# Optimization experiments

Hardware: AMD Instinct MI355X
Metric: run time of the kernel (lower is better)

The kernel has to match this reference:

```python
import jax, jax.numpy as jnp
import numpy as np

B = 4           # batchsize == poolsize, pool = arange(B)
N_NODES = 32768
N_EDGES = 262144
CH_V = 16
CH_E = 16
HID = 64
CH_MSG = 2 * CH_V + CH_E  # 48


def setup_inputs() -> dict:
    key = jax.random.key(0)
    ks = jax.random.split(key, 8)
    node_vals = jax.random.normal(ks[0], (B, N_NODES, CH_V), jnp.float32) * 0.01
    edge_vals = jax.random.normal(ks[1], (B, N_EDGES, CH_E), jnp.float32) * 0.1
    conn_a = jax.random.randint(ks[2], (N_EDGES,), 0, N_NODES)
    conn_b = jax.random.randint(ks[3], (N_EDGES,), 0, N_NODES)
    w = lambda k, sh: jax.random.normal(k, sh, jnp.float32) * 0.1
    return {
        "node_vals": node_vals, "edge_vals": edge_vals,
        "conn_a": conn_a, "conn_b": conn_b,
        "Wm1": w(ks[4], (CH_MSG, HID)), "bm1": jnp.zeros((HID,), jnp.float32),
        "Wm2": w(ks[5], (HID, CH_MSG)), "bm2": jnp.zeros((CH_MSG,), jnp.float32),
        "Wu1": w(ks[6], (3 * CH_V, HID)), "bu1": jnp.zeros((HID,), jnp.float32),
        "Wu2": w(ks[7], (HID, CH_V)), "bu2": jnp.zeros((CH_V,), jnp.float32),
    }


def reference(node_vals, edge_vals, conn_a, conn_b,
              Wm1, bm1, Wm2, bm2, Wu1, bu1, Wu2, bu2):
    # NeuralGraph.timestep with node_dropout_p = edge_dropout_p = 0 (masks are identity),
    # use_update=True, average_messages=True, nodes=True, edges=True.
    h_a = node_vals[:, conn_a]                      # [B, E, CH_V] gather at source nodes
    h_b = node_vals[:, conn_b]                      # [B, E, CH_V] gather at target nodes
    h = jnp.concatenate([h_a, h_b, edge_vals], -1)  # [B, E, 48]
    # message MLP (Linear -> tanh -> Linear)
    m = jnp.tanh(h @ Wm1 + bm1) @ Wm2 + bm2         # [B, E, 48]
    m_a = m[..., :CH_V]
    m_b = m[..., CH_V:2 * CH_V]
    m_ab = m[..., 2 * CH_V:]
    # scatter-add aggregation per node (index_add_ along node dim)
    agg_a = jnp.zeros((B, N_NODES, CH_V), m.dtype).at[:, conn_a].add(m_a)
    agg_b = jnp.zeros((B, N_NODES, CH_V), m.dtype).at[:, conn_b].add(m_b)
    # count-based averaging (counts clamped to >= 1, matching the buffer fixup)
    ones = jnp.ones((N_EDGES,), m.dtype)
    cnt_a = jnp.maximum(jax.ops.segment_sum(ones, conn_a, num_segments=N_NODES), 1.0)
    cnt_b = jnp.maximum(jax.ops.segment_sum(ones, conn_b, num_segments=N_NODES), 1.0)
    agg_a = agg_a / cnt_a[None, :, None]
    agg_b = agg_b / cnt_b[None, :, None]
    # update MLP
    u_in = jnp.concatenate([agg_a, agg_b, node_vals], -1)   # [B, N, 48]
    updates = jnp.tanh(u_in @ Wu1 + bu1) @ Wu2 + bu2        # [B, N, CH_V]
    new_node_vals = node_vals + updates
    new_edge_vals = edge_vals + m_ab
    return new_node_vals, new_edge_vals
```

## Files before the change

kernel.cpp:

```cpp
#include <hip/hip_runtime.h>
#include <hip/hip_bf16.h>
#include <cstdint>
#include <cstddef>

#define B 4
#define NN 32768
#define NE 262144
#define CV 16
#define CE 16
#define HID 64
#define CM 48

using frag  = __attribute__((ext_vector_type(8))) short;
using f32x4 = __attribute__((ext_vector_type(4))) float;

__device__ __forceinline__ float fast_tanh(float x) {
    float e = __expf(2.0f * x);
    return 1.0f - 2.0f / (e + 1.0f);
}

__device__ __forceinline__ unsigned short f2bf(float x) {
    union { float f; unsigned u; } v; v.f = x;
    unsigned r = (v.u + 0x7FFFu + ((v.u >> 16) & 1u)) >> 16;
    return (unsigned short)r;
}

__device__ __forceinline__ float bf2f(unsigned short x) {
    union { unsigned u; float f; } v; v.u = ((unsigned)x) << 16;
    return v.f;
}

__device__ __forceinline__ unsigned pk2bf(float lo, float hi) {
    union { __hip_bfloat162 h; unsigned u; } v;
    v.h = __float22bfloat162_rn(make_float2(lo, hi));
    return v.u;
}

__device__ __forceinline__ unsigned swo(int row, int byte_off) {
    return (unsigned)((row << 7) + (byte_off ^ ((row & 7) << 4)));
}

__device__ __forceinline__ void acc8(float* a, uint4 v) {
    a[0] += bf2f((unsigned short)(v.x & 0xFFFFu));
    a[1] += bf2f((unsigned short)(v.x >> 16));
    a[2] += bf2f((unsigned short)(v.y & 0xFFFFu));
    a[3] += bf2f((unsigned short)(v.y >> 16));
    a[4] += bf2f((unsigned short)(v.z & 0xFFFFu));
    a[5] += bf2f((unsigned short)(v.z >> 16));
    a[6] += bf2f((unsigned short)(v.w & 0xFFFFu));
    a[7] += bf2f((unsigned short)(v.w >> 16));
}

__global__ __launch_bounds__(256) void count_kernel(
    const int* __restrict__ ca, const int* __restrict__ cb,
    int* __restrict__ cnt_a, int* __restrict__ cnt_b,
    int* __restrict__ rank_a, int* __restrict__ rank_b,
    const float* __restrict__ Wm1, const float* __restrict__ bm1,
    const float* __restrict__ Wm2,
    const float* __restrict__ Wu1, const float* __restrict__ bu1,
    const float* __restrict__ Wu2,
    const float* __restrict__ node_vals,
    unsigned short* __restrict__ pW1, unsigned short* __restrict__ pW2,
    unsigned short* __restrict__ pWu1, unsigned short* __restrict__ pWu2,
    unsigned short* __restrict__ nv16)
{
    int i = blockIdx.x * 256 + threadIdx.x;
    rank_a[i] = atomicAdd(&cnt_a[ca[i]], 1);
    rank_b[i] = atomicAdd(&cnt_b[cb[i]], 1);

    {
        int x0 = i * 8;
        const float4* src = (const float4*)(node_vals + x0);
        float4 v0 = src[0], v1 = src[1];
        uint4 o;
        o.x = pk2bf(v0.x, v0.y); o.y = pk2bf(v0.z, v0.w);
        o.z = pk2bf(v1.x, v1.y); o.w = pk2bf(v1.z, v1.w);
        *(uint4*)(nv16 + x0) = o;
    }

    if (blockIdx.x == 0) {
        for (int x = threadIdx.x; x < 4 * 2 * 64 * 8; x += 256) {
            int j = x & 7, lane = (x >> 3) & 63, ks = (x >> 9) & 1, mt = x >> 10;
            int m = mt * 16 + (lane & 15);
            int k = ks * 32 + (lane >> 4) * 8 + j;
            float w = (k < 48) ? Wm1[k * 64 + m] : (k == 48 ? bm1[m] : 0.0f);
            pW1[x] = f2bf(w);
        }
    } else if (blockIdx.x == 1) {
        for (int x = threadIdx.x; x < 3 * 2 * 64 * 8; x += 256) {
            int j = x & 7, lane = (x >> 3) & 63, ks = (x >> 9) & 1, mt = x >> 10;
            int m = mt * 16 + (lane & 15);
            int k = ks * 32 + (lane >> 4) * 8 + j;
            pW2[x] = f2bf(Wm2[k * 48 + m]);
        }
    } else if (blockIdx.x == 2) {
        for (int x = threadIdx.x; x < 4 * 2 * 64 * 8; x += 256) {
            int j = x & 7, lane = (x >> 3) & 63, ks = (x >> 9) & 1, mt = x >> 10;
            int m = mt * 16 + (lane & 15);
            int k = ks * 32 + (lane >> 4) * 8 + j;
            float w = (k < 48) ? Wu1[k * 64 + m] : (k == 48 ? bu1[m] : 0.0f);
            pWu1[x] = f2bf(w);
        }
    } else if (blockIdx.x == 3) {
        for (int x = threadIdx.x; x < 2 * 64 * 8; x += 256) {
            int j = x & 7, lane = (x >> 3) & 63, ks = x >> 9;
            int m = lane & 15;
            int k = ks * 32 + (lane >> 4) * 8 + j;
            pWu2[x] = f2bf(Wu2[k * 16 + m]);
        }
    }
}

__global__ __launch_bounds__(1024) void scan_kernel(
    const int* __restrict__ cnt_a, int* __restrict__ start_a,
    const int* __restrict__ cnt_b, int* __restrict__ start_b)
{
    const int* cnt = (blockIdx.x == 0) ? cnt_a : cnt_b;
    int* start     = (blockIdx.x == 0) ? start_a : start_b;

    __shared__ int sw[16];
    int t = threadIdx.x;
    int lane = t & 63;
    int wv   = t >> 6;
    int base = t * 32;

    int local[32];
    int sum = 0;
    const int4* p = (const int4*)(cnt + base);
#pragma unroll
    for (int q = 0; q < 8; q++) {
        int4 v = p[q];
        local[q*4+0] = v.x; local[q*4+1] = v.y; local[q*4+2] = v.z; local[q*4+3] = v.w;
        sum += v.x + v.y + v.z + v.w;
    }
    int inc = sum;
#pragma unroll
    for (int off = 1; off < 64; off <<= 1) {
        int u = __shfl_up(inc, off);
        if (lane >= off) inc += u;
    }
    if (lane == 63) sw[wv] = inc;
    __syncthreads();
    if (wv == 0 && lane < 16) {
        int v = sw[lane];
        int i2 = v;
#pragma unroll
        for (int off = 1; off < 16; off <<= 1) {
            int u = __shfl_up(i2, off);
            if (lane >= off) i2 += u;
        }
        sw[lane] = i2 - v;
    }
    __syncthreads();

    int run = sw[wv] + inc - sum;
    int4* ps = (int4*)(start + base);
#pragma unroll
    for (int q = 0; q < 8; q++) {
        int4 o;
        o.x = run; run += local[q*4+0];
        o.y = run; run += local[q*4+1];
        o.z = run; run += local[q*4+2];
        o.w = run; run += local[q*4+3];
        ps[q] = o;
    }
}

__global__ __launch_bounds__(256) void eidx_kernel(
    const int* __restrict__ ca, const int* __restrict__ cb,
    const int* __restrict__ rank_a, const int* __restrict__ rank_b,
    const int* __restrict__ start_a, const int* __restrict__ start_b,
    int* __restrict__ eidx_a, int* __restrict__ eidx_b)
{
    int e = blockIdx.x * 256 + threadIdx.x;
    eidx_a[start_a[ca[e]] + rank_a[e]] = e;
    eidx_b[start_b[cb[e]] + rank_b[e]] = e;
}

__global__ __launch_bounds__(256, 5) void edge_kernel(
    const unsigned short* __restrict__ nv16, const float* __restrict__ edge_vals,
    const int* __restrict__ ca, const int* __restrict__ cb,
    const unsigned short* __restrict__ pW1, const unsigned short* __restrict__ pW2,
    const float* __restrict__ bm2,
    float* __restrict__ out_edge,
    unsigned short* __restrict__ ma, unsigned short* __restrict__ mb)
{
    __shared__ unsigned short sH[256 * 64];
    char* sB = (char*)sH;

    int t    = threadIdx.x;
    int lane = t & 63;
    int col  = lane & 15;
    int quad = lane >> 4;
    int erow = (t >> 6) * 64;
    int cha  = quad * 4;

    size_t eb  = (size_t)blockIdx.x * 256;
    size_t idx = eb + t;
    int e  = (int)(idx & (NE - 1));
    int bb = (int)(idx >> 18);

    int na = ca[e], nb = cb[e];

    {
        const uint4* gA = (const uint4*)(nv16 + ((size_t)bb * NN + na) * CV);
        const uint4* gB = (const uint4*)(nv16 + ((size_t)bb * NN + nb) * CV);
        uint4 a0 = gA[0], a1 = gA[1];
        uint4 b0 = gB[0], b1 = gB[1];
        const float4* pE = (const float4*)(edge_vals + idx * CE);
        float4 ev0 = pE[0], ev1 = pE[1], ev2 = pE[2], ev3 = pE[3];

        unsigned pk[32];
        *(uint4*)&pk[0]  = a0;  *(uint4*)&pk[4]  = a1;
        *(uint4*)&pk[8]  = b0;  *(uint4*)&pk[12] = b1;
        pk[16] = pk2bf(ev0.x, ev0.y); pk[17] = pk2bf(ev0.z, ev0.w);
        pk[18] = pk2bf(ev1.x, ev1.y); pk[19] = pk2bf(ev1.z, ev1.w);
        pk[20] = pk2bf(ev2.x, ev2.y); pk[21] = pk2bf(ev2.z, ev2.w);
        pk[22] = pk2bf(ev3.x, ev3.y); pk[23] = pk2bf(ev3.z, ev3.w);
        pk[24] = 0x3F80u;
#pragma unroll
        for (int q = 25; q < 32; q++) pk[q] = 0;
        const uint4* src = (const uint4*)pk;
#pragma unroll
        for (int q = 0; q < 8; q++)
            *(uint4*)(sB + swo(t, q * 16)) = src[q];
    }
    asm volatile("s_waitcnt lgkmcnt(0)" ::: "memory");

#pragma unroll
    for (int hh = 0; hh < 2; hh++) {
        int r0 = erow + hh * 32 + col;

        frag w1f[4][2];
#pragma unroll
        for (int mt = 0; mt < 4; mt++)
#pragma unroll
            for (int ks = 0; ks < 2; ks++)
                w1f[mt][ks] = *(const frag*)&pW1[(((mt * 2 + ks) * 64) + lane) * 8];

        f32x4 acc1[4][2];
#pragma unroll
        for (int mt = 0; mt < 4; mt++)
#pragma unroll
            for (int n = 0; n < 2; n++) acc1[mt][n] = (f32x4){0.f, 0.f, 0.f, 0.f};

#pragma unroll
        for (int ks = 0; ks < 2; ks++) {
            frag bfr[2];
#pragma unroll
            for (int n = 0; n < 2; n++)
                bfr[n] = *(const frag*)(sB + swo(r0 + n * 16, ks * 64 + quad * 16));
#pragma unroll
            for (int mt = 0; mt < 4; mt++)
#pragma unroll
                for (int n = 0; n < 2; n++)
                    acc1[mt][n] = __builtin_amdgcn_mfma_f32_16x16x32_bf16(
                        w1f[mt][ks], bfr[n], acc1[mt][n], 0, 0, 0);
        }

#pragma unroll
        for (int n = 0; n < 2; n++) {
            int row = r0 + n * 16;
#pragma unroll
            for (int mt = 0; mt < 4; mt++) {
                uint2 w;
                w.x = pk2bf(fast_tanh(acc1[mt][n][0]), fast_tanh(acc1[mt][n][1]));
                w.y = pk2bf(fast_tanh(acc1[mt][n][2]), fast_tanh(acc1[mt][n][3]));
                *(uint2*)(sB + swo(row, mt * 32 + quad * 8)) = w;
            }
        }
        asm volatile("s_waitcnt lgkmcnt(0)" ::: "memory");

        frag w2f[3][2];
#pragma unroll
        for (int mt = 0; mt < 3; mt++)
#pragma unroll
            for (int ks = 0; ks < 2; ks++)
                w2f[mt][ks] = *(const frag*)&pW2[(((mt * 2 + ks) * 64) + lane) * 8];

        f32x4 acc2[3][2];
#pragma unroll
        for (int mt = 0; mt < 3; mt++)
#pragma unroll
            for (int n = 0; n < 2; n++) acc2[mt][n] = (f32x4){0.f, 0.f, 0.f, 0.f};

#pragma unroll
        for (int ks = 0; ks < 2; ks++) {
            frag bfr[2];
#pragma unroll
            for (int n = 0; n < 2; n++)
                bfr[n] = *(const frag*)(sB + swo(r0 + n * 16, ks * 64 + quad * 16));
#pragma unroll
            for (int mt = 0; mt < 3; mt++)
#pragma unroll
                for (int n = 0; n < 2; n++)
                    acc2[mt][n] = __builtin_amdgcn_mfma_f32_16x16x32_bf16(
                        w2f[mt][ks], bfr[n], acc2[mt][n], 0, 0, 0);
        }

        float4 b2e = *(const float4*)&bm2[32 + cha];
#pragma unroll
        for (int n = 0; n < 2; n++) {
            int le = r0 + n * 16;
            size_t o = (eb + le) * CE + cha;
            float4 evv = *(const float4*)&edge_vals[o];
            float4 ov;
            ov.x = evv.x + acc2[2][n][0] + b2e.x;
            ov.y = evv.y + acc2[2][n][1] + b2e.y;
            ov.z = evv.z + acc2[2][n][2] + b2e.z;
            ov.w = evv.w + acc2[2][n][3] + b2e.w;
            *(float4*)&out_edge[o] = ov;
        }

        float4 b2a = *(const float4*)&bm2[cha];
        float4 b2b = *(const float4*)&bm2[16 + cha];
#pragma unroll
        for (int n = 0; n < 2; n++) {
            int row = r0 + n * 16;
            uint2 wa;
            wa.x = pk2bf(acc2[0][n][0] + b2a.x, acc2[0][n][1] + b2a.y);
            wa.y = pk2bf(acc2[0][n][2] + b2a.z, acc2[0][n][3] + b2a.w);
            *(uint2*)(sB + swo(row, quad * 8)) = wa;
            uint2 wb;
            wb.x = pk2bf(acc2[1][n][0] + b2b.x, acc2[1][n][1] + b2b.y);
            wb.y = pk2bf(acc2[1][n][2] + b2b.z, acc2[1][n][3] + b2b.w);
            *(uint2*)(sB + swo(row, 32 + quad * 8)) = wb;
        }
    }
    asm volatile("s_waitcnt lgkmcnt(0)" ::: "memory");

    {
        uint4 a0 = *(const uint4*)(sB + swo(t, 0));
        uint4 a1 = *(const uint4*)(sB + swo(t, 16));
        uint4 b0 = *(const uint4*)(sB + swo(t, 32));
        uint4 b1 = *(const uint4*)(sB + swo(t, 48));
        unsigned short* pa = &ma[idx * 16];
        *(uint4*)(pa + 0) = a0;
        *(uint4*)(pa + 8) = a1;
        unsigned short* pb = &mb[idx * 16];
        *(uint4*)(pb + 0) = b0;
        *(uint4*)(pb + 8) = b1;
    }
}

__global__ __launch_bounds__(256, 4) void node_kernel(
    const float* __restrict__ node_vals,
    const unsigned short* __restrict__ ma, const unsigned short* __restrict__ mb,
    const int* __restrict__ eidx_a, const int* __restrict__ eidx_b,
    const int* __restrict__ start_a, const int* __restrict__ start_b,
    const int* __restrict__ cnt_a, const int* __restrict__ cnt_b,
    const unsigned short* __restrict__ pWu1, const unsigned short* __restrict__ pWu2,
    const float* __restrict__ bu2,
    float* __restrict__ out_node)
{
    __shared__ unsigned short sH[256 * 64];
    char* sB = (char*)sH;

    int t    = threadIdx.x;
    int lane = t & 63;
    int col  = lane & 15;
    int quad = lane >> 4;
    int erow = (t >> 6) * 64;

    int g = blockIdx.x * 256 + t;
    int n = g & (NN - 1);
    int b = g >> 15;

    float4 pn[4];
    {
        float ua[16] = {0.f,0.f,0.f,0.f,0.f,0.f,0.f,0.f,0.f,0.f,0.f,0.f,0.f,0.f,0.f,0.f};
        float ub[16] = {0.f,0.f,0.f,0.f,0.f,0.f,0.f,0.f,0.f,0.f,0.f,0.f,0.f,0.f,0.f,0.f};
        int da = cnt_a[n], sa = start_a[n];
        int db = cnt_b[n], sbn = start_b[n];
        const int* ia = eidx_a + sa;
        const int* ib = eidx_b + sbn;
        const unsigned short* mab = ma + (size_t)b * NE * 16;
        const unsigned short* mbb = mb + (size_t)b * NE * 16;
        int kmax = max(da, db);
        for (int k = 0; k < kmax; k++) {
            if (k < da) {
                int ee = ia[k];
                const uint4* p = (const uint4*)(mab + (size_t)ee * 16);
                uint4 v0 = p[0], v1 = p[1];
                acc8(&ua[0], v0);
                acc8(&ua[8], v1);
            }
            if (k < db) {
                int ee = ib[k];
                const uint4* p = (const uint4*)(mbb + (size_t)ee * 16);
                uint4 v0 = p[0], v1 = p[1];
                acc8(&ub[0], v0);
                acc8(&ub[8], v1);
            }
        }
        float inva = 1.0f / (float)max(da, 1);
        float invb = 1.0f / (float)max(db, 1);

        const float4* pnv = (const float4*)(node_vals + (size_t)g * CV);
#pragma unroll
        for (int q = 0; q < 4; q++) pn[q] = pnv[q];

        unsigned pk[32];
#pragma unroll
        for (int q = 0; q < 8; q++)
            pk[q] = pk2bf(ua[2*q] * inva, ua[2*q+1] * inva);
#pragma unroll
        for (int q = 0; q < 8; q++)
            pk[8 + q] = pk2bf(ub[2*q] * invb, ub[2*q+1] * invb);
#pragma unroll
        for (int q = 0; q < 4; q++) {
            pk[16 + 2*q + 0] = pk2bf(pn[q].x, pn[q].y);
            pk[16 + 2*q + 1] = pk2bf(pn[q].z, pn[q].w);
        }
        pk[24] = 0x3F80u;
#pragma unroll
        for (int q = 25; q < 32; q++) pk[q] = 0;
        const uint4* src = (const uint4*)pk;
#pragma unroll
        for (int q = 0; q < 8; q++)
            *(uint4*)(sB + swo(t, q * 16)) = src[q];
    }
    asm volatile("s_waitcnt lgkmcnt(0)" ::: "memory");

#pragma unroll
    for (int hh = 0; hh < 2; hh++) {
        int r0 = erow + hh * 32 + col;

        frag w1f[4][2];
#pragma unroll
        for (int mt = 0; mt < 4; mt++)
#pragma unroll
            for (int ks = 0; ks < 2; ks++)
                w1f[mt][ks] = *(const frag*)&pWu1[(((mt * 2 + ks) * 64) + lane) * 8];

        f32x4 acc1[4][2];
#pragma unroll
        for (int mt = 0; mt < 4; mt++)
#pragma unroll
            for (int nt = 0; nt < 2; nt++) acc1[mt][nt] = (f32x4){0.f, 0.f, 0.f, 0.f};

#pragma unroll
        for (int ks = 0; ks < 2; ks++) {
            frag bfr[2];
#pragma unroll
            for (int nt = 0; nt < 2; nt++)
                bfr[nt] = *(const frag*)(sB + swo(r0 + nt * 16, ks * 64 + quad * 16));
#pragma unroll
            for (int mt = 0; mt < 4; mt++)
#pragma unroll
                for (int nt = 0; nt < 2; nt++)
                    acc1[mt][nt] = __builtin_amdgcn_mfma_f32_16x16x32_bf16(
                        w1f[mt][ks], bfr[nt], acc1[mt][nt], 0, 0, 0);
        }

#pragma unroll
        for (int nt = 0; nt < 2; nt++) {
            int row = r0 + nt * 16;
#pragma unroll
            for (int mt = 0; mt < 4; mt++) {
                uint2 w;
                w.x = pk2bf(fast_tanh(acc1[mt][nt][0]), fast_tanh(acc1[mt][nt][1]));
                w.y = pk2bf(fast_tanh(acc1[mt][nt][2]), fast_tanh(acc1[mt][nt][3]));
                *(uint2*)(sB + swo(row, mt * 32 + quad * 8)) = w;
            }
        }
        asm volatile("s_waitcnt lgkmcnt(0)" ::: "memory");

        frag w2f[2];
#pragma unroll
        for (int ks = 0; ks < 2; ks++)
            w2f[ks] = *(const frag*)&pWu2[(ks * 64 + lane) * 8];

        f32x4 acc2[2];
#pragma unroll
        for (int nt = 0; nt < 2; nt++) acc2[nt] = (f32x4){0.f, 0.f, 0.f, 0.f};

#pragma unroll
        for (int ks = 0; ks < 2; ks++) {
            frag bfr[2];
#pragma unroll
            for (int nt = 0; nt < 2; nt++)
                bfr[nt] = *(const frag*)(sB + swo(r0 + nt * 16, ks * 64 + quad * 16));
#pragma unroll
            for (int nt = 0; nt < 2; nt++)
                acc2[nt] = __builtin_amdgcn_mfma_f32_16x16x32_bf16(
                    w2f[ks], bfr[nt], acc2[nt], 0, 0, 0);
        }

#pragma unroll
        for (int nt = 0; nt < 2; nt++) {
            int row = r0 + nt * 16;
            float4 v;
            v.x = acc2[nt][0]; v.y = acc2[nt][1];
            v.z = acc2[nt][2]; v.w = acc2[nt][3];
            *(float4*)(sB + swo(row, 64 + quad * 16)) = v;
        }
    }
    asm volatile("s_waitcnt lgkmcnt(0)" ::: "memory");

    {
        const float4* pb2 = (const float4*)bu2;
        float4* po = (float4*)&out_node[(size_t)g * CV];
#pragma unroll
        for (int q = 0; q < 4; q++) {
            float4 m = *(const float4*)(sB + swo(t, 64 + q * 16));
            float4 c = pb2[q];
            float4 o;
            o.x = pn[q].x + m.x + c.x;
            o.y = pn[q].y + m.y + c.y;
            o.z = pn[q].z + m.z + c.z;
            o.w = pn[q].w + m.w + c.w;
            po[q] = o;
        }
    }
}

extern "C" void kernel_launch(void* const* d_in, const int* in_sizes, int n_in,
                              void* d_out, int out_size, void* d_ws, size_t ws_size,
                              hipStream_t stream) {
    const float* node_vals = (const float*)d_in[0];
    const float* edge_vals = (const float*)d_in[1];
    const int*   ca        = (const int*)d_in[2];
    const int*   cb        = (const int*)d_in[3];
    const float* Wm1 = (const float*)d_in[4];
    const float* bm1 = (const float*)d_in[5];
    const float* Wm2 = (const float*)d_in[6];
    const float* bm2 = (const float*)d_in[7];
    const float* Wu1 = (const float*)d_in[8];
    const float* bu1 = (const float*)d_in[9];
    const float* Wu2 = (const float*)d_in[10];
    const float* bu2 = (const float*)d_in[11];

    float* out_node = (float*)d_out;
    float* out_edge = out_node + (size_t)B * NN * CV;

    unsigned short* ma = (unsigned short*)d_ws;
    unsigned short* mb = ma + (size_t)B * NE * 16;
    int* cnt_a   = (int*)(mb + (size_t)B * NE * 16);
    int* cnt_b   = cnt_a + NN;
    int* start_a = cnt_b + NN;
    int* start_b = start_a + NN;
    int* rank_a  = start_b + NN;
    int* rank_b  = rank_a + NE;
    int* eidx_a  = rank_b + NE;
    int* eidx_b  = eidx_a + NE;
    unsigned short* pW1  = (unsigned short*)(eidx_b + NE);
    unsigned short* pW2  = pW1 + 4096;
    unsigned short* pWu1 = pW2 + 3072;
    unsigned short* pWu2 = pWu1 + 4096;
    unsigned short* nv16 = pWu2 + 1024;

    hipMemsetAsync(cnt_a, 0, 2 * (size_t)NN * sizeof(int), stream);

    count_kernel<<<NE / 256, 256, 0, stream>>>(
        ca, cb, cnt_a, cnt_b, rank_a, rank_b,
        Wm1, bm1, Wm2, Wu1, bu1, Wu2, node_vals,
        pW1, pW2, pWu1, pWu2, nv16);
    scan_kernel<<<2, 1024, 0, stream>>>(cnt_a, start_a, cnt_b, start_b);
    eidx_kernel<<<NE / 256, 256, 0, stream>>>(
        ca, cb, rank_a, rank_b, start_a, start_b, eidx_a, eidx_b);
    edge_kernel<<<(B * NE) / 256, 256, 0, stream>>>(
        nv16, edge_vals, ca, cb, pW1, pW2, bm2, out_edge, ma, mb);
    node_kernel<<<(B * NN) / 256, 256, 0, stream>>>(
        node_vals, ma, mb, eidx_a, eidx_b, start_a, start_b, cnt_a, cnt_b,
        pWu1, pWu2, bu2, out_node);
}
```

Before: 284.6 us.

## Fuse count, scan and index build into one cooperative kernel; batch node gathers

The count, prefix-scan and edge-index kernels are merged into a single cooperative kernel that uses grid-wide syncs. Ranks now stay in registers instead of going through global rank arrays. The scan is run by two 256-thread blocks, each handling 128 counts per thread, and the node kernel loads up to four neighbour messages before accumulating them, to expose more memory-level parallelism. The node kernel also drops its minimum-occupancy launch bound. Risks: a cooperative launch of 1024 blocks needs all blocks co-resident, and the scan is now serialized through only two blocks while the rest of the grid waits.

```diff
diff --git a/kernel.cpp b/kernel.cpp
--- a/kernel.cpp
+++ b/kernel.cpp
@@ -1,7 +1,10 @@
 #include <hip/hip_runtime.h>
 #include <hip/hip_bf16.h>
+#include <hip/hip_cooperative_groups.h>
 #include <cstdint>
 #include <cstddef>
+
+namespace cg = cooperative_groups;
 
 #define B 4
 #define NN 32768
@@ -51,10 +54,11 @@
     a[7] += bf2f((unsigned short)(v.w >> 16));
 }
 
-__global__ __launch_bounds__(256) void count_kernel(
+__global__ __launch_bounds__(256) void pre_kernel(
     const int* __restrict__ ca, const int* __restrict__ cb,
     int* __restrict__ cnt_a, int* __restrict__ cnt_b,
-    int* __restrict__ rank_a, int* __restrict__ rank_b,
+    int* __restrict__ start_a, int* __restrict__ start_b,
+    int* __restrict__ eidx_a, int* __restrict__ eidx_b,
     const float* __restrict__ Wm1, const float* __restrict__ bm1,
     const float* __restrict__ Wm2,
     const float* __restrict__ Wu1, const float* __restrict__ bu1,
@@ -64,12 +68,19 @@
     unsigned short* __restrict__ pWu1, unsigned short* __restrict__ pWu2,
     unsigned short* __restrict__ nv16)
 {
-    int i = blockIdx.x * 256 + threadIdx.x;
-    rank_a[i] = atomicAdd(&cnt_a[ca[i]], 1);
-    rank_b[i] = atomicAdd(&cnt_b[cb[i]], 1);
+    cg::grid_group grid = cg::this_grid();
+    __shared__ int sw[4];
+
+    int t   = threadIdx.x;
+    int bid = blockIdx.x;
+    int e   = bid * 256 + t;
+
+    int na = ca[e], nb = cb[e];
+    int ra = atomicAdd(&cnt_a[na], 1);
+    int rb = atomicAdd(&cnt_b[nb], 1);
 
     {
-        int x0 = i * 8;
+        int x0 = e * 8;
         const float4* src = (const float4*)(node_vals + x0);
         float4 v0 = src[0], v1 = src[1];
         uint4 o;
@@ -78,103 +89,78 @@
         *(uint4*)(nv16 + x0) = o;
     }
 
-    if (blockIdx.x == 0) {
-        for (int x = threadIdx.x; x < 4 * 2 * 64 * 8; x += 256) {
+    if (bid == 0) {
+        for (int x = t; x < 4 * 2 * 64 * 8; x += 256) {
             int j = x & 7, lane = (x >> 3) & 63, ks = (x >> 9) & 1, mt = x >> 10;
             int m = mt * 16 + (lane & 15);
             int k = ks * 32 + (lane >> 4) * 8 + j;
             float w = (k < 48) ? Wm1[k * 64 + m] : (k == 48 ? bm1[m] : 0.0f);
             pW1[x] = f2bf(w);
         }
-    } else if (blockIdx.x == 1) {
-        for (int x = threadIdx.x; x < 3 * 2 * 64 * 8; x += 256) {
+    } else if (bid == 1) {
+        for (int x = t; x < 3 * 2 * 64 * 8; x += 256) {
             int j = x & 7, lane = (x >> 3) & 63, ks = (x >> 9) & 1, mt = x >> 10;
             int m = mt * 16 + (lane & 15);
             int k = ks * 32 + (lane >> 4) * 8 + j;
             pW2[x] = f2bf(Wm2[k * 48 + m]);
         }
-    } else if (blockIdx.x == 2) {
-        for (int x = threadIdx.x; x < 4 * 2 * 64 * 8; x += 256) {
+    } else if (bid == 2) {
+        for (int x = t; x < 4 * 2 * 64 * 8; x += 256) {
             int j = x & 7, lane = (x >> 3) & 63, ks = (x >> 9) & 1, mt = x >> 10;
             int m = mt * 16 + (lane & 15);
             int k = ks * 32 + (lane >> 4) * 8 + j;
             float w = (k < 48) ? Wu1[k * 64 + m] : (k == 48 ? bu1[m] : 0.0f);
             pWu1[x] = f2bf(w);
         }
-    } else if (blockIdx.x == 3) {
-        for (int x = threadIdx.x; x < 2 * 64 * 8; x += 256) {
+    } else if (bid == 3) {
+        for (int x = t; x < 2 * 64 * 8; x += 256) {
             int j = x & 7, lane = (x >> 3) & 63, ks = x >> 9;
             int m = lane & 15;
             int k = ks * 32 + (lane >> 4) * 8 + j;
             pWu2[x] = f2bf(Wu2[k * 16 + m]);
         }
     }
-}
-
-__global__ __launch_bounds__(1024) void scan_kernel(
-    const int* __restrict__ cnt_a, int* __restrict__ start_a,
-    const int* __restrict__ cnt_b, int* __restrict__ start_b)
-{
-    const int* cnt = (blockIdx.x == 0) ? cnt_a : cnt_b;
-    int* start     = (blockIdx.x == 0) ? start_a : start_b;
-
-    __shared__ int sw[16];
-    int t = threadIdx.x;
-    int lane = t & 63;
-    int wv   = t >> 6;
-    int base = t * 32;
-
-    int local[32];
-    int sum = 0;
-    const int4* p = (const int4*)(cnt + base);
-#pragma unroll
-    for (int q = 0; q < 8; q++) {
-        int4 v = p[q];
-        local[q*4+0] = v.x; local[q*4+1] = v.y; local[q*4+2] = v.z; local[q*4+3] = v.w;
-        sum += v.x + v.y + v.z + v.w;
-    }
-    int inc = sum;
-#pragma unroll
-    for (int off = 1; off < 64; off <<= 1) {
-        int u = __shfl_up(inc, off);
-        if (lane >= off) inc += u;
-    }
-    if (lane == 63) sw[wv] = inc;
-    __syncthreads();
-    if (wv == 0 && lane < 16) {
-        int v = sw[lane];
-        int i2 = v;
-#pragma unroll
-        for (int off = 1; off < 16; off <<= 1) {
-            int u = __shfl_up(i2, off);
-            if (lane >= off) i2 += u;
-        }
-        sw[lane] = i2 - v;
-    }
-    __syncthreads();
-
-    int run = sw[wv] + inc - sum;
-    int4* ps = (int4*)(start + base);
-#pragma unroll
-    for (int q = 0; q < 8; q++) {
-        int4 o;
-        o.x = run; run += local[q*4+0];
-        o.y = run; run += local[q*4+1];
-        o.z = run; run += local[q*4+2];
-        o.w = run; run += local[q*4+3];
-        ps[q] = o;
-    }
-}
-
-__global__ __launch_bounds__(256) void eidx_kernel(
-    const int* __restrict__ ca, const int* __restrict__ cb,
-    const int* __restrict__ rank_a, const int* __restrict__ rank_b,
-    const int* __restrict__ start_a, const int* __restrict__ start_b,
-    int* __restrict__ eidx_a, int* __restrict__ eidx_b)
-{
-    int e = blockIdx.x * 256 + threadIdx.x;
-    eidx_a[start_a[ca[e]] + rank_a[e]] = e;
-    eidx_b[start_b[cb[e]] + rank_b[e]] = e;
+
+    grid.sync();
+
+    if (bid < 2) {
+        const int* cnt = (bid == 0) ? cnt_a : cnt_b;
+        int* start     = (bid == 0) ? start_a : start_b;
+        int lane = t & 63;
+        int wv   = t >> 6;
+        int base = t * 128;
+        const int4* p = (const int4*)(cnt + base);
+        int sum = 0;
+#pragma unroll
+        for (int q = 0; q < 32; q++) { int4 v = p[q]; sum += v.x + v.y + v.z + v.w; }
+        int inc = sum;
+#pragma unroll
+        for (int off = 1; off < 64; off <<= 1) {
+            int u = __shfl_up(inc, off);
+            if (lane >= off) inc += u;
+        }
+        if (lane == 63) sw[wv] = inc;
+        __syncthreads();
+        int woff = 0;
+        for (int w = 0; w < wv; w++) woff += sw[w];
+        int run = woff + inc - sum;
+        int4* ps = (int4*)(start + base);
+#pragma unroll
+        for (int q = 0; q < 32; q++) {
+            int4 v = p[q];
+            int4 o;
+            o.x = run; run += v.x;
+            o.y = run; run += v.y;
+            o.z = run; run += v.z;
+            o.w = run; run += v.w;
+            ps[q] = o;
+        }
+    }
+
+    grid.sync();
+
+    eidx_a[start_a[na] + ra] = e;
+    eidx_b[start_b[nb] + rb] = e;
 }
 
 __global__ __launch_bounds__(256, 5) void edge_kernel(
@@ -343,7 +329,7 @@
     }
 }
 
-__global__ __launch_bounds__(256, 4) void node_kernel(
+__global__ __launch_bounds__(256) void node_kernel(
     const float* __restrict__ node_vals,
     const unsigned short* __restrict__ ma, const unsigned short* __restrict__ mb,
     const int* __restrict__ eidx_a, const int* __restrict__ eidx_b,
@@ -377,20 +363,27 @@
         const unsigned short* mab = ma + (size_t)b * NE * 16;
         const unsigned short* mbb = mb + (size_t)b * NE * 16;
         int kmax = max(da, db);
-        for (int k = 0; k < kmax; k++) {
-            if (k < da) {
-                int ee = ia[k];
-                const uint4* p = (const uint4*)(mab + (size_t)ee * 16);
-                uint4 v0 = p[0], v1 = p[1];
-                acc8(&ua[0], v0);
-                acc8(&ua[8], v1);
+        for (int k0 = 0; k0 < kmax; k0 += 4) {
+            uint4 av[4][2], bv[4][2];
+            int na_ = da - k0; na_ = (na_ < 0) ? 0 : ((na_ > 4) ? 4 : na_);
+            int nb_ = db - k0; nb_ = (nb_ < 0) ? 0 : ((nb_ > 4) ? 4 : nb_);
+#pragma unroll
+            for (int j = 0; j < 4; j++) {
+                if (j < na_) {
+                    int ee = ia[k0 + j];
+                    const uint4* p = (const uint4*)(mab + (size_t)ee * 16);
+                    av[j][0] = p[0]; av[j][1] = p[1];
+                }
+                if (j < nb_) {
+                    int ee = ib[k0 + j];
+                    const uint4* p = (const uint4*)(mbb + (size_t)ee * 16);
+                    bv[j][0] = p[0]; bv[j][1] = p[1];
+                }
             }
-            if (k < db) {
-                int ee = ib[k];
-                const uint4* p = (const uint4*)(mbb + (size_t)ee * 16);
-                uint4 v0 = p[0], v1 = p[1];
-                acc8(&ub[0], v0);
-                acc8(&ub[8], v1);
+#pragma unroll
+            for (int j = 0; j < 4; j++) {
+                if (j < na_) { acc8(&ua[0], av[j][0]); acc8(&ua[8], av[j][1]); }
+                if (j < nb_) { acc8(&ub[0], bv[j][0]); acc8(&ub[8], bv[j][1]); }
             }
         }
         float inva = 1.0f / (float)max(da, 1);
@@ -540,9 +533,7 @@
     int* cnt_b   = cnt_a + NN;
     int* start_a = cnt_b + NN;
     int* start_b = start_a + NN;
-    int* rank_a  = start_b + NN;
-    int* rank_b  = rank_a + NE;
-    int* eidx_a  = rank_b + NE;
+    int* eidx_a  = start_b + NN;
     int* eidx_b  = eidx_a + NE;
     unsigned short* pW1  = (unsigned short*)(eidx_b + NE);
     unsigned short* pW2  = pW1 + 4096;
@@ -552,13 +543,22 @@
 
     hipMemsetAsync(cnt_a, 0, 2 * (size_t)NN * sizeof(int), stream);
 
-    count_kernel<<<NE / 256, 256, 0, stream>>>(
-        ca, cb, cnt_a, cnt_b, rank_a, rank_b,
-        Wm1, bm1, Wm2, Wu1, bu1, Wu2, node_vals,
-        pW1, pW2, pWu1, pWu2, nv16);
-    scan_kernel<<<2, 1024, 0, stream>>>(cnt_a, start_a, cnt_b, start_b);
-    eidx_kernel<<<NE / 256, 256, 0, stream>>>(
-        ca, cb, rank_a, rank_b, start_a, start_b, eidx_a, eidx_b);
+    {
+        void* args[] = {
+            (void*)&ca, (void*)&cb,
+            (void*)&cnt_a, (void*)&cnt_b,
+            (void*)&start_a, (void*)&start_b,
+            (void*)&eidx_a, (void*)&eidx_b,
+            (void*)&Wm1, (void*)&bm1, (void*)&Wm2,
+            (void*)&Wu1, (void*)&bu1, (void*)&Wu2,
+            (void*)&node_vals,
+            (void*)&pW1, (void*)&pW2, (void*)&pWu1, (void*)&pWu2,
+            (void*)&nv16
+        };
+        hipLaunchCooperativeKernel((void*)pre_kernel, dim3(NE / 256), dim3(256),
+                                   args, 0, stream);
+    }
+
     edge_kernel<<<(B * NE) / 256, 256, 0, stream>>>(
         nv16, edge_vals, ca, cb, pW1, pW2, bm2, out_edge, ma, mb);
     node_kernel<<<(B * NN) / 256, 256, 0, stream>>>(
```

Measured after the change: 499.4 us. +75.5%, slower.

## Split node gather across two thread halves and batch edge loads by four

Applied to the files above, without the earlier changes.

The node kernel now runs 512 threads per block. One half of the threads aggregates the source-side (a) messages and the other half the target-side (b) messages, instead of a single thread doing both sequentially. Each gather loop issues up to four edge-message loads before accumulating them, which adds memory-level parallelism. The MLP phase spreads its row bands across 8 waves, and block-level barriers replace the wave-local waitcnt. The cost is more threads, two __syncthreads, and higher register pressure from the batched loads.

```diff
diff --git a/kernel.cpp b/kernel.cpp
--- a/kernel.cpp
+++ b/kernel.cpp
@@ -343,7 +343,7 @@
     }
 }
 
-__global__ __launch_bounds__(256, 4) void node_kernel(
+__global__ __launch_bounds__(512) void node_kernel(
     const float* __restrict__ node_vals,
     const unsigned short* __restrict__ ma, const unsigned short* __restrict__ mb,
     const int* __restrict__ eidx_a, const int* __restrict__ eidx_b,
@@ -357,74 +357,75 @@
     char* sB = (char*)sH;
 
     int t    = threadIdx.x;
-    int lane = t & 63;
-    int col  = lane & 15;
-    int quad = lane >> 4;
-    int erow = (t >> 6) * 64;
-
-    int g = blockIdx.x * 256 + t;
+    int tn   = t & 255;
+    int half = t >> 8;
+    int g = blockIdx.x * 256 + tn;
     int n = g & (NN - 1);
     int b = g >> 15;
 
     float4 pn[4];
+
     {
-        float ua[16] = {0.f,0.f,0.f,0.f,0.f,0.f,0.f,0.f,0.f,0.f,0.f,0.f,0.f,0.f,0.f,0.f};
-        float ub[16] = {0.f,0.f,0.f,0.f,0.f,0.f,0.f,0.f,0.f,0.f,0.f,0.f,0.f,0.f,0.f,0.f};
-        int da = cnt_a[n], sa = start_a[n];
-        int db = cnt_b[n], sbn = start_b[n];
-        const int* ia = eidx_a + sa;
-        const int* ib = eidx_b + sbn;
-        const unsigned short* mab = ma + (size_t)b * NE * 16;
-        const unsigned short* mbb = mb + (size_t)b * NE * 16;
-        int kmax = max(da, db);
-        for (int k = 0; k < kmax; k++) {
-            if (k < da) {
-                int ee = ia[k];
-                const uint4* p = (const uint4*)(mab + (size_t)ee * 16);
-                uint4 v0 = p[0], v1 = p[1];
-                acc8(&ua[0], v0);
-                acc8(&ua[8], v1);
+        const int* cntp = half ? cnt_b : cnt_a;
+        const int* stp  = half ? start_b : start_a;
+        const int* ep   = half ? eidx_b : eidx_a;
+        const unsigned short* mp = (half ? mb : ma) + (size_t)b * NE * 16;
+
+        int d = cntp[n], s = stp[n];
+        const int* ix = ep + s;
+
+        float u[16] = {0.f,0.f,0.f,0.f,0.f,0.f,0.f,0.f,0.f,0.f,0.f,0.f,0.f,0.f,0.f,0.f};
+        for (int k0 = 0; k0 < d; k0 += 4) {
+            uint4 v[4][2];
+            int nn_ = d - k0; nn_ = (nn_ > 4) ? 4 : nn_;
+#pragma unroll
+            for (int j = 0; j < 4; j++) {
+                if (j < nn_) {
+                    int ee = ix[k0 + j];
+                    const uint4* p = (const uint4*)(mp + (size_t)ee * 16);
+                    v[j][0] = p[0]; v[j][1] = p[1];
+                }
             }
-            if (k < db) {
-                int ee = ib[k];
-                const uint4* p = (const uint4*)(mbb + (size_t)ee * 16);
-                uint4 v0 = p[0], v1 = p[1];
-                acc8(&ub[0], v0);
-                acc8(&ub[8], v1);
+#pragma unroll
+            for (int j = 0; j < 4; j++) {
+                if (j < nn_) { acc8(&u[0], v[j][0]); acc8(&u[8], v[j][1]); }
             }
         }
-        float inva = 1.0f / (float)max(da, 1);
-        float invb = 1.0f / (float)max(db, 1);
-
-        const float4* pnv = (const float4*)(node_vals + (size_t)g * CV);
-#pragma unroll
-        for (int q = 0; q < 4; q++) pn[q] = pnv[q];
-
-        unsigned pk[32];
-#pragma unroll
-        for (int q = 0; q < 8; q++)
-            pk[q] = pk2bf(ua[2*q] * inva, ua[2*q+1] * inva);
-#pragma unroll
-        for (int q = 0; q < 8; q++)
-            pk[8 + q] = pk2bf(ub[2*q] * invb, ub[2*q+1] * invb);
-#pragma unroll
-        for (int q = 0; q < 4; q++) {
-            pk[16 + 2*q + 0] = pk2bf(pn[q].x, pn[q].y);
-            pk[16 + 2*q + 1] = pk2bf(pn[q].z, pn[q].w);
-        }
-        pk[24] = 0x3F80u;
-#pragma unroll
-        for (int q = 25; q < 32; q++) pk[q] = 0;
-        const uint4* src = (const uint4*)pk;
-#pragma unroll
-        for (int q = 0; q < 8; q++)
-            *(uint4*)(sB + swo(t, q * 16)) = src[q];
-    }
-    asm volatile("s_waitcnt lgkmcnt(0)" ::: "memory");
-
-#pragma unroll
-    for (int hh = 0; hh < 2; hh++) {
-        int r0 = erow + hh * 32 + col;
+        float inv = 1.0f / (float)max(d, 1);
+        unsigned pk[8];
+#pragma unroll
+        for (int q = 0; q < 8; q++) pk[q] = pk2bf(u[2*q] * inv, u[2*q+1] * inv);
+        *(uint4*)(sB + swo(tn, half * 32 + 0))  = ((const uint4*)pk)[0];
+        *(uint4*)(sB + swo(tn, half * 32 + 16)) = ((const uint4*)pk)[1];
+
+        if (half == 0) {
+            const float4* pnv = (const float4*)(node_vals + (size_t)g * CV);
+#pragma unroll
+            for (int q = 0; q < 4; q++) pn[q] = pnv[q];
+            unsigned pk2[16];
+#pragma unroll
+            for (int q = 0; q < 4; q++) {
+                pk2[2*q + 0] = pk2bf(pn[q].x, pn[q].y);
+                pk2[2*q + 1] = pk2bf(pn[q].z, pn[q].w);
+            }
+            pk2[8] = 0x3F80u;
+#pragma unroll
+            for (int q = 9; q < 16; q++) pk2[q] = 0;
+#pragma unroll
+            for (int q = 0; q < 4; q++)
+                *(uint4*)(sB + swo(tn, 64 + q * 16)) = ((const uint4*)pk2)[q];
+        }
+    }
+    __syncthreads();
+
+    {
+        int lane = t & 63;
+        int col  = lane & 15;
+        int quad = lane >> 4;
+        int wv   = t >> 6;
+        int band = wv & 3;
+        int hh   = wv >> 2;
+        int r0 = band * 64 + hh * 32 + col;
 
         frag w1f[4][2];
 #pragma unroll
@@ -496,14 +497,14 @@
             *(float4*)(sB + swo(row, 64 + quad * 16)) = v;
         }
     }
-    asm volatile("s_waitcnt lgkmcnt(0)" ::: "memory");
-
-    {
+    __syncthreads();
+
+    if (half == 0) {
         const float4* pb2 = (const float4*)bu2;
         float4* po = (float4*)&out_node[(size_t)g * CV];
 #pragma unroll
         for (int q = 0; q < 4; q++) {
-            float4 m = *(const float4*)(sB + swo(t, 64 + q * 16));
+            float4 m = *(const float4*)(sB + swo(tn, 64 + q * 16));
             float4 c = pb2[q];
             float4 o;
             o.x = pn[q].x + m.x + c.x;
@@ -561,7 +562,7 @@
         ca, cb, rank_a, rank_b, start_a, start_b, eidx_a, eidx_b);
     edge_kernel<<<(B * NE) / 256, 256, 0, stream>>>(
         nv16, edge_vals, ca, cb, pW1, pW2, bm2, out_edge, ma, mb);
-    node_kernel<<<(B * NN) / 256, 256, 0, stream>>>(
+    node_kernel<<<(B * NN) / 256, 512, 0, stream>>>(
         node_vals, ma, mb, eidx_a, eidx_b, start_a, start_b, cnt_a, cnt_b,
         pWu1, pWu2, bu2, out_node);
 }
```

Result: no change. 280.8 us (-1.3%).
